# Kernel tuning notes

Measured on AMD Instinct MI355X. Metric: run time of the kernel, lower is better.

Reference implementation:

```python
import jax, jax.numpy as jnp
import numpy as np

D_MODEL = 512
N_HEADS = 8
D_HEAD = D_MODEL // N_HEADS  # 64


def setup_inputs() -> dict:
    key = jax.random.key(0)
    ks = jax.random.split(key, 9)
    S = 4096
    sc_qkv = 1.0 / np.sqrt(D_MODEL)
    x = jax.random.normal(ks[0], (S, D_MODEL), dtype=jnp.float32)
    # per-head projection weights, stacked over heads: [H, D_MODEL, D_HEAD]
    Wq = jax.random.normal(ks[1], (N_HEADS, D_MODEL, D_HEAD), dtype=jnp.float32) * sc_qkv
    Wk = jax.random.normal(ks[2], (N_HEADS, D_MODEL, D_HEAD), dtype=jnp.float32) * sc_qkv
    Wv = jax.random.normal(ks[3], (N_HEADS, D_MODEL, D_HEAD), dtype=jnp.float32) * sc_qkv
    bq = jax.random.normal(ks[4], (N_HEADS, D_HEAD), dtype=jnp.float32) * 0.01
    bk = jax.random.normal(ks[5], (N_HEADS, D_HEAD), dtype=jnp.float32) * 0.01
    bv = jax.random.normal(ks[6], (N_HEADS, D_HEAD), dtype=jnp.float32) * 0.01
    # output projection (nn.Linear(512,512)): weight [out,in], bias [out]
    Wo = jax.random.normal(ks[7], (D_MODEL, D_MODEL), dtype=jnp.float32) * sc_qkv
    bo = jax.random.normal(ks[8], (D_MODEL,), dtype=jnp.float32) * 0.01
    return {"x": x, "Wq": Wq, "Wk": Wk, "Wv": Wv, "bq": bq, "bk": bk, "bv": bv, "Wo": Wo, "bo": bo}


def reference(x, Wq, Wk, Wv, bq, bk, bv, Wo, bo):
    # x: [S, D_MODEL]; all heads batched in one einsum (replaces python loop)
    q = jnp.einsum('sd,hdk->hsk', x, Wq) + bq[:, None, :]  # [H,S,Dh]
    k = jnp.einsum('sd,hdk->hsk', x, Wk) + bk[:, None, :]
    v = jnp.einsum('sd,hdk->hsk', x, Wv) + bv[:, None, :]
    scale = 1.0 / jnp.sqrt(jnp.asarray(D_HEAD, dtype=q.dtype))
    scores = jnp.einsum('hsk,htk->hst', q, k) * scale  # [H,S,S]
    attn = jax.nn.softmax(scores, axis=-1)
    ctx = jnp.einsum('hst,htk->hsk', attn, v)  # [H,S,Dh]
    # concat heads along feature dim: [S, H*Dh] (head-major order matches torch.concat)
    S = x.shape[0]
    concat = jnp.transpose(ctx, (1, 0, 2)).reshape(S, N_HEADS * D_HEAD)
    # nn.Linear: y = x @ W^T + b
    return concat @ Wo.T + bo
```

## Files before the change

kernel.cpp:

```cpp
#include <hip/hip_runtime.h>

#define S 4096
#define DM 512
#define NH 8
#define DHD 64
#define KVSPLIT 2
#define KVLEN (S / KVSPLIT)
#define ALPHA 0.18033688011112042f

using short8 = __attribute__((ext_vector_type(8))) short;
using f32x4  = __attribute__((ext_vector_type(4))) float;

__device__ __forceinline__ unsigned short f2bf(float f) {
  union { float f; unsigned int u; } v; v.f = f;
  unsigned int r = v.u + 0x7FFF + ((v.u >> 16) & 1);
  return (unsigned short)(r >> 16);
}

__device__ __forceinline__ float bf2f(unsigned short u) {
  union { unsigned int u; float f; } v; v.u = (unsigned)u << 16;
  return v.f;
}

__device__ __forceinline__ unsigned int cvt_pk_bf16(float a, float b) {
  unsigned int r;
  asm("v_cvt_pk_bf16_f32 %0, %1, %2" : "=v"(r) : "v"(a), "v"(b));
  return r;
}

__device__ __forceinline__ void async16(void* lds, const void* g) {
  __builtin_amdgcn_global_load_lds((const __attribute__((address_space(1))) void*)g,
                                   (__attribute__((address_space(3))) void*)lds, 16, 0, 0);
}

__global__ void cvt2_f32_bf16(const float* __restrict__ a, unsigned short* __restrict__ da, int na,
                              const float* __restrict__ b, unsigned short* __restrict__ db, int nb) {
  int i = (blockIdx.x * 256 + threadIdx.x) * 4;
  const float* src; unsigned short* dst;
  if (i < na) { src = a + i; dst = da + i; }
  else { int j = i - na; if (j >= nb) return; src = b + j; dst = db + j; }
  float4 v = *(const float4*)src;
  uint2 o;
  o.x = (unsigned)f2bf(v.x) | ((unsigned)f2bf(v.y) << 16);
  o.y = (unsigned)f2bf(v.z) | ((unsigned)f2bf(v.w) << 16);
  *(uint2*)dst = o;
}

__global__ void pack_w(const float* __restrict__ Wq, const float* __restrict__ Wk,
                       const float* __restrict__ Wv, unsigned short* __restrict__ Wcat) {
  __shared__ float T[64][68];
  const int d0 = blockIdx.x * 64, h = blockIdx.y, t = blockIdx.z;
  const float* W = (t == 0 ? Wq : t == 1 ? Wk : Wv) + (size_t)h * DM * DHD;
  const int tid = threadIdx.x;
#pragma unroll
  for (int i = 0; i < 4; ++i) {
    int c = i * 256 + tid;
    int r = c >> 4, u = c & 15;
    *(float4*)&T[r][u * 4] = *(const float4*)&W[(size_t)(d0 + r) * DHD + u * 4];
  }
  __syncthreads();
#pragma unroll
  for (int i = 0; i < 2; ++i) {
    int c = i * 256 + tid;
    int dh = c >> 3, u = c & 7;
    unsigned short tmp[8];
#pragma unroll
    for (int j = 0; j < 8; ++j) tmp[j] = f2bf(T[u * 8 + j][dh]);
    *(uint4*)&Wcat[((size_t)(t * 512) + h * 64 + dh) * DM + d0 + u * 8] = *(uint4*)tmp;
  }
}

template <int EPI>
__global__ void __launch_bounds__(256, 2)
gemm_bt(const unsigned short* __restrict__ A,
        const unsigned short* __restrict__ B,
        int K,
        const float* __restrict__ b0, const float* __restrict__ b1, const float* __restrict__ b2,
        unsigned short* __restrict__ Qb, unsigned short* __restrict__ Kb, unsigned short* __restrict__ Vtb,
        float* __restrict__ outp) {
  __shared__ unsigned short As[128 * 32];
  __shared__ unsigned short Bs[128 * 32];
  const int tid = threadIdx.x;
  const int wid = tid >> 6, lane = tid & 63;
  const int lo = lane & 15, hi = lane >> 4;
  const int wr = wid >> 1, wc = wid & 1;
  const int m0 = blockIdx.x * 128, n0 = blockIdx.y * 128;
  f32x4 acc[4][4] = {};
  for (int k0 = 0; k0 < K; k0 += 32) {
    __syncthreads();
#pragma unroll
    for (int i = 0; i < 2; ++i) {
      const int cb = (wid * 2 + i) * 64;
      const int c = cb + lane;
      const int r = c >> 2, u = c & 3;
      async16(&As[cb * 8], A + (size_t)(m0 + r) * K + k0 + u * 8);
      async16(&Bs[cb * 8], B + (size_t)(n0 + r) * K + k0 + u * 8);
    }
    __syncthreads();
    short8 af[4], bfr[4];
#pragma unroll
    for (int m = 0; m < 4; ++m) af[m] = *(const short8*)&As[(wr * 64 + m * 16 + lo) * 32 + hi * 8];
#pragma unroll
    for (int n = 0; n < 4; ++n) bfr[n] = *(const short8*)&Bs[(wc * 64 + n * 16 + lo) * 32 + hi * 8];
#pragma unroll
    for (int m = 0; m < 4; ++m)
#pragma unroll
      for (int n = 0; n < 4; ++n)
        acc[m][n] = __builtin_amdgcn_mfma_f32_16x16x32_bf16(af[m], bfr[n], acc[m][n], 0, 0, 0);
  }
#pragma unroll
  for (int mi = 0; mi < 4; ++mi)
#pragma unroll
    for (int ni = 0; ni < 4; ++ni) {
      const int n = n0 + wc * 64 + ni * 16 + lo;
      const int mbase = m0 + wr * 64 + mi * 16 + hi * 4;
      if (EPI == 0) {
        const int t = n >> 9, h = (n >> 6) & 7, dh = n & 63;
        const float bias = (t == 0 ? b0 : t == 1 ? b1 : b2)[h * 64 + dh];
        if (t == 2) {
          unsigned short tmp[4];
#pragma unroll
          for (int r = 0; r < 4; ++r) tmp[r] = f2bf(acc[mi][ni][r] + bias);
          *(uint2*)&Vtb[((size_t)h * DHD + dh) * S + mbase] = *(uint2*)tmp;
        } else {
          unsigned short* dst = (t == 0 ? Qb : Kb);
#pragma unroll
          for (int r = 0; r < 4; ++r) {
            float v = acc[mi][ni][r] + bias;
            if (t == 0) v *= ALPHA;
            dst[((size_t)h * S + mbase + r) * DHD + dh] = f2bf(v);
          }
        }
      } else {
#pragma unroll
        for (int r = 0; r < 4; ++r)
          outp[(size_t)(mbase + r) * DM + n] = acc[mi][ni][r] + b0[n];
      }
    }
}

__global__ void __launch_bounds__(256, 4)
attn_kernel(const unsigned short* __restrict__ Qb, const unsigned short* __restrict__ Kb,
            const unsigned short* __restrict__ Vtb, unsigned short* __restrict__ accP,
            float2* __restrict__ lmP) {
  __shared__ unsigned short Ks[2][64 * 64];
  __shared__ unsigned short Vs[2][64 * 64];
  __shared__ unsigned short Ps[4][16 * 64];
  const int tid = threadIdx.x;
  const int wid = tid >> 6, lane = tid & 63;
  const int lo = lane & 15, hi = lane >> 4;
  const int h = blockIdx.y;
  const int q0 = blockIdx.x * 64;
  const int sp = blockIdx.z;
  const int kvbase = sp * KVLEN;
  const unsigned short* Qh  = Qb  + (size_t)h * S * DHD;
  const unsigned short* Kh  = Kb  + (size_t)h * S * DHD;
  const unsigned short* Vth = Vtb + (size_t)h * DHD * S;
  const int qrow = q0 + wid * 16 + lo;
  short8 qf[2];
#pragma unroll
  for (int kf = 0; kf < 2; ++kf)
    qf[kf] = *(const short8*)&Qh[(size_t)qrow * DHD + kf * 32 + hi * 8];

  float m_r = -__builtin_inff(), l_r = 0.f;
  f32x4 acc[4] = {};

  auto stage = [&](int b, int kv0) {
#pragma unroll
    for (int i = 0; i < 2; ++i) {
      const int cb = (wid * 2 + i) * 64;
      const int c = cb + lane;
      const int r = c >> 3, up = c & 7;
      const int u = up ^ (r & 7);
      async16(&Ks[b][cb * 8], Kh  + (size_t)(kv0 + r) * DHD + u * 8);
      async16(&Vs[b][cb * 8], Vth + (size_t)r * S + kv0 + u * 8);
    }
  };

  stage(0, kvbase);
  __syncthreads();
  int cur = 0;
  for (int kv0 = kvbase; kv0 < kvbase + KVLEN; kv0 += 64) {
    if (kv0 + 64 < kvbase + KVLEN) stage(cur ^ 1, kv0 + 64);
    f32x4 sc[4];
    __builtin_amdgcn_s_setprio(1);
#pragma unroll
    for (int ct = 0; ct < 4; ++ct) {
      sc[ct] = (f32x4){0.f, 0.f, 0.f, 0.f};
#pragma unroll
      for (int kf = 0; kf < 2; ++kf) {
        const int r = ct * 16 + lo;
        const int u = kf * 4 + hi;
        const short8 kfr = *(const short8*)&Ks[cur][r * 64 + (u ^ (r & 7)) * 8];
        sc[ct] = __builtin_amdgcn_mfma_f32_16x16x32_bf16(kfr, qf[kf], sc[ct], 0, 0, 0);
      }
    }
    __builtin_amdgcn_s_setprio(0);
    float pm = fmaxf(fmaxf(fmaxf(sc[0][0], sc[0][1]), fmaxf(sc[0][2], sc[0][3])),
                     fmaxf(fmaxf(sc[1][0], sc[1][1]), fmaxf(sc[1][2], sc[1][3])));
    pm = fmaxf(pm, fmaxf(fmaxf(fmaxf(sc[2][0], sc[2][1]), fmaxf(sc[2][2], sc[2][3])),
                         fmaxf(fmaxf(sc[3][0], sc[3][1]), fmaxf(sc[3][2], sc[3][3]))));
    pm = fmaxf(pm, __shfl_xor(pm, 16));
    pm = fmaxf(pm, __shfl_xor(pm, 32));
    if (__any(pm > m_r + 8.f)) {
      const float mn = fmaxf(m_r, pm);
      const float sca = exp2f(m_r - mn);
      m_r = mn;
      l_r *= sca;
#pragma unroll
      for (int dt = 0; dt < 4; ++dt)
#pragma unroll
        for (int r = 0; r < 4; ++r) acc[dt][r] *= sca;
    }
    float ps = 0.f;
#pragma unroll
    for (int ct = 0; ct < 4; ++ct)
#pragma unroll
      for (int r = 0; r < 4; ++r) {
        const float p = exp2f(sc[ct][r] - m_r);
        sc[ct][r] = p;
        ps += p;
      }
    ps += __shfl_xor(ps, 16);
    ps += __shfl_xor(ps, 32);
    l_r += ps;
    unsigned short* Pw = &Ps[wid][0];
    const int swz = (lo & 7) << 3;
#pragma unroll
    for (int ct = 0; ct < 4; ++ct) {
      uint2 w;
      w.x = cvt_pk_bf16(sc[ct][0], sc[ct][1]);
      w.y = cvt_pk_bf16(sc[ct][2], sc[ct][3]);
      *(uint2*)&Pw[lo * 64 + ((ct * 16 + hi * 4) ^ swz)] = w;
    }
    asm volatile("" ::: "memory");
    short8 pb[2];
#pragma unroll
    for (int kc = 0; kc < 2; ++kc)
      pb[kc] = *(const short8*)&Pw[lo * 64 + ((kc * 32 + hi * 8) ^ swz)];
    __builtin_amdgcn_s_setprio(1);
#pragma unroll
    for (int dt = 0; dt < 4; ++dt)
#pragma unroll
      for (int kc = 0; kc < 2; ++kc) {
        const int r2 = dt * 16 + lo;
        const int u = kc * 4 + hi;
        const short8 vf = *(const short8*)&Vs[cur][r2 * 64 + (u ^ (r2 & 7)) * 8];
        acc[dt] = __builtin_amdgcn_mfma_f32_16x16x32_bf16(vf, pb[kc], acc[dt], 0, 0, 0);
      }
    __builtin_amdgcn_s_setprio(0);
    __syncthreads();
    cur ^= 1;
  }
  const size_t prow = (size_t)(sp * NH + h) * S + qrow;
#pragma unroll
  for (int dt = 0; dt < 4; ++dt) {
    unsigned short tmp[4];
#pragma unroll
    for (int r = 0; r < 4; ++r) tmp[r] = f2bf(acc[dt][r]);
    *(uint2*)&accP[prow * 64 + dt * 16 + hi * 4] = *(uint2*)tmp;
  }
  if (hi == 0) lmP[prow] = make_float2(m_r, l_r);
}

__global__ void merge_kernel(const unsigned short* __restrict__ accP, const float2* __restrict__ lmP,
                             unsigned short* __restrict__ concat) {
  const int c = blockIdx.x * 256 + threadIdx.x;
  const int row = c >> 3;
  const int h = row >> 12, q = row & (S - 1);
  const int dh0 = (c & 7) * 8;
  const float2 lm0 = lmP[row];
  const float2 lm1 = lmP[NH * S + row];
  const float M = fmaxf(lm0.x, lm1.x);
  float w0 = exp2f(lm0.x - M), w1 = exp2f(lm1.x - M);
  const float inv = 1.f / (lm0.y * w0 + lm1.y * w1);
  w0 *= inv; w1 *= inv;
  const short8 v0 = *(const short8*)&accP[(size_t)row * 64 + dh0];
  const short8 v1 = *(const short8*)&accP[((size_t)NH * S + row) * 64 + dh0];
  unsigned short out[8];
#pragma unroll
  for (int j = 0; j < 8; ++j)
    out[j] = f2bf(bf2f((unsigned short)v0[j]) * w0 + bf2f((unsigned short)v1[j]) * w1);
  *(uint4*)&concat[(size_t)q * DM + h * DHD + dh0] = *(uint4*)out;
}

extern "C" void kernel_launch(void* const* d_in, const int* in_sizes, int n_in,
                              void* d_out, int out_size, void* d_ws, size_t ws_size,
                              hipStream_t stream) {
  const float* x  = (const float*)d_in[0];
  const float* Wq = (const float*)d_in[1];
  const float* Wk = (const float*)d_in[2];
  const float* Wv = (const float*)d_in[3];
  const float* bq = (const float*)d_in[4];
  const float* bk = (const float*)d_in[5];
  const float* bv = (const float*)d_in[6];
  const float* Wo = (const float*)d_in[7];
  const float* bo = (const float*)d_in[8];
  float* outp = (float*)d_out;
  char* ws = (char*)d_ws;
  unsigned short* Qbuf   = (unsigned short*)(ws + 0);
  unsigned short* Kbuf   = (unsigned short*)(ws + 4194304);
  unsigned short* Vtbuf  = (unsigned short*)(ws + 8388608);
  unsigned short* concat = (unsigned short*)(ws + 12582912);
  unsigned short* Wob    = (unsigned short*)(ws + 16777216);
  float2*         lmP    = (float2*)(ws + 17301504);
  unsigned short* xb     = (unsigned short*)(ws + 17825792);
  unsigned short* Wcat   = (unsigned short*)(ws + 22020096);
  unsigned short* accP   = (unsigned short*)(ws + 17825792);

  cvt2_f32_bf16<<<(S * DM + DM * DM) / 1024, 256, 0, stream>>>(x, xb, S * DM, Wo, Wob, DM * DM);
  pack_w<<<dim3(8, NH, 3), 256, 0, stream>>>(Wq, Wk, Wv, Wcat);
  gemm_bt<0><<<dim3(S / 128, 1536 / 128), 256, 0, stream>>>(xb, Wcat, DM, bq, bk, bv,
                                                            Qbuf, Kbuf, Vtbuf, nullptr);
  attn_kernel<<<dim3(S / 64, NH, KVSPLIT), 256, 0, stream>>>(Qbuf, Kbuf, Vtbuf, accP, lmP);
  merge_kernel<<<(NH * S * 8) / 256, 256, 0, stream>>>(accP, lmP, concat);
  gemm_bt<1><<<dim3(S / 128, DM / 128), 256, 0, stream>>>(concat, Wob, DM, bo, nullptr, nullptr,
                                                          nullptr, nullptr, nullptr, outp);
}
```

Measured before the change: 184.6 us.

## Switch attention to 32x32 MFMA with in-register P, fuse prep kernels, narrow GEMM tiles

The attention kernel moves from 16x16x32 to 32x32x16 bf16 MFMA tiles with 128 query rows per block. The P matrix is repacked in registers with v_permlane32_swap instead of going through LDS, which removes the per-wave LDS staging and its traffic. The two preprocessing kernels are merged into one launch, and the GEMM N-tile is halved to 64 with higher occupancy bounds to get more blocks in flight. The trade-offs are higher register pressure in attention (launch bounds lowered to 2) and less data reuse per GEMM tile.

```diff
diff --git a/kernel.cpp b/kernel.cpp
--- a/kernel.cpp
+++ b/kernel.cpp
@@ -10,6 +10,7 @@
 
 using short8 = __attribute__((ext_vector_type(8))) short;
 using f32x4  = __attribute__((ext_vector_type(4))) float;
+using f32x16 = __attribute__((ext_vector_type(16))) float;
 
 __device__ __forceinline__ unsigned short f2bf(float f) {
   union { float f; unsigned int u; } v; v.f = f;
@@ -28,30 +29,37 @@
   return r;
 }
 
+__device__ __forceinline__ void permswap(unsigned int& d, unsigned int& s) {
+  asm("v_permlane32_swap_b32 %0, %1" : "+v"(d), "+v"(s));
+}
+
 __device__ __forceinline__ void async16(void* lds, const void* g) {
   __builtin_amdgcn_global_load_lds((const __attribute__((address_space(1))) void*)g,
                                    (__attribute__((address_space(3))) void*)lds, 16, 0, 0);
 }
 
-__global__ void cvt2_f32_bf16(const float* __restrict__ a, unsigned short* __restrict__ da, int na,
-                              const float* __restrict__ b, unsigned short* __restrict__ db, int nb) {
-  int i = (blockIdx.x * 256 + threadIdx.x) * 4;
-  const float* src; unsigned short* dst;
-  if (i < na) { src = a + i; dst = da + i; }
-  else { int j = i - na; if (j >= nb) return; src = b + j; dst = db + j; }
-  float4 v = *(const float4*)src;
-  uint2 o;
-  o.x = (unsigned)f2bf(v.x) | ((unsigned)f2bf(v.y) << 16);
-  o.y = (unsigned)f2bf(v.z) | ((unsigned)f2bf(v.w) << 16);
-  *(uint2*)dst = o;
-}
-
-__global__ void pack_w(const float* __restrict__ Wq, const float* __restrict__ Wk,
-                       const float* __restrict__ Wv, unsigned short* __restrict__ Wcat) {
+#define NCVT ((S * DM + DM * DM) / 1024)
+__global__ void prep(const float* __restrict__ x, unsigned short* __restrict__ xb,
+                     const float* __restrict__ Wo, unsigned short* __restrict__ Wob,
+                     const float* __restrict__ Wq, const float* __restrict__ Wk,
+                     const float* __restrict__ Wv, unsigned short* __restrict__ Wcat) {
   __shared__ float T[64][68];
-  const int d0 = blockIdx.x * 64, h = blockIdx.y, t = blockIdx.z;
+  const int tid = threadIdx.x;
+  if (blockIdx.x < NCVT) {
+    int i = (blockIdx.x * 256 + tid) * 4;
+    const float* src; unsigned short* dst;
+    if (i < S * DM) { src = x + i; dst = xb + i; }
+    else { int j = i - S * DM; src = Wo + j; dst = Wob + j; }
+    float4 v = *(const float4*)src;
+    uint2 o;
+    o.x = (unsigned)f2bf(v.x) | ((unsigned)f2bf(v.y) << 16);
+    o.y = (unsigned)f2bf(v.z) | ((unsigned)f2bf(v.w) << 16);
+    *(uint2*)dst = o;
+    return;
+  }
+  const int bid = blockIdx.x - NCVT;
+  const int d0 = (bid & 7) * 64, h = (bid >> 3) & 7, t = bid >> 6;
   const float* W = (t == 0 ? Wq : t == 1 ? Wk : Wv) + (size_t)h * DM * DHD;
-  const int tid = threadIdx.x;
 #pragma unroll
   for (int i = 0; i < 4; ++i) {
     int c = i * 256 + tid;
@@ -71,7 +79,7 @@
 }
 
 template <int EPI>
-__global__ void __launch_bounds__(256, 2)
+__global__ void __launch_bounds__(256, 4)
 gemm_bt(const unsigned short* __restrict__ A,
         const unsigned short* __restrict__ B,
         int K,
@@ -79,40 +87,43 @@
         unsigned short* __restrict__ Qb, unsigned short* __restrict__ Kb, unsigned short* __restrict__ Vtb,
         float* __restrict__ outp) {
   __shared__ unsigned short As[128 * 32];
-  __shared__ unsigned short Bs[128 * 32];
+  __shared__ unsigned short Bs[64 * 32];
   const int tid = threadIdx.x;
   const int wid = tid >> 6, lane = tid & 63;
   const int lo = lane & 15, hi = lane >> 4;
   const int wr = wid >> 1, wc = wid & 1;
-  const int m0 = blockIdx.x * 128, n0 = blockIdx.y * 128;
-  f32x4 acc[4][4] = {};
+  const int m0 = blockIdx.x * 128, n0 = blockIdx.y * 64;
+  f32x4 acc[4][2] = {};
   for (int k0 = 0; k0 < K; k0 += 32) {
     __syncthreads();
 #pragma unroll
     for (int i = 0; i < 2; ++i) {
       const int cb = (wid * 2 + i) * 64;
-      const int c = cb + lane;
-      const int r = c >> 2, u = c & 3;
+      const int c = cb + lane, r = c >> 2, u = c & 3;
       async16(&As[cb * 8], A + (size_t)(m0 + r) * K + k0 + u * 8);
+    }
+    {
+      const int cb = wid * 64;
+      const int c = cb + lane, r = c >> 2, u = c & 3;
       async16(&Bs[cb * 8], B + (size_t)(n0 + r) * K + k0 + u * 8);
     }
     __syncthreads();
-    short8 af[4], bfr[4];
+    short8 af[4], bfr[2];
 #pragma unroll
     for (int m = 0; m < 4; ++m) af[m] = *(const short8*)&As[(wr * 64 + m * 16 + lo) * 32 + hi * 8];
 #pragma unroll
-    for (int n = 0; n < 4; ++n) bfr[n] = *(const short8*)&Bs[(wc * 64 + n * 16 + lo) * 32 + hi * 8];
+    for (int n = 0; n < 2; ++n) bfr[n] = *(const short8*)&Bs[(wc * 32 + n * 16 + lo) * 32 + hi * 8];
 #pragma unroll
     for (int m = 0; m < 4; ++m)
 #pragma unroll
-      for (int n = 0; n < 4; ++n)
+      for (int n = 0; n < 2; ++n)
         acc[m][n] = __builtin_amdgcn_mfma_f32_16x16x32_bf16(af[m], bfr[n], acc[m][n], 0, 0, 0);
   }
 #pragma unroll
   for (int mi = 0; mi < 4; ++mi)
 #pragma unroll
-    for (int ni = 0; ni < 4; ++ni) {
-      const int n = n0 + wc * 64 + ni * 16 + lo;
+    for (int ni = 0; ni < 2; ++ni) {
+      const int n = n0 + wc * 32 + ni * 16 + lo;
       const int mbase = m0 + wr * 64 + mi * 16 + hi * 4;
       if (EPI == 0) {
         const int t = n >> 9, h = (n >> 6) & 7, dh = n & 63;
@@ -139,41 +150,39 @@
     }
 }
 
-__global__ void __launch_bounds__(256, 4)
+__global__ void __launch_bounds__(256, 2)
 attn_kernel(const unsigned short* __restrict__ Qb, const unsigned short* __restrict__ Kb,
             const unsigned short* __restrict__ Vtb, unsigned short* __restrict__ accP,
             float2* __restrict__ lmP) {
   __shared__ unsigned short Ks[2][64 * 64];
   __shared__ unsigned short Vs[2][64 * 64];
-  __shared__ unsigned short Ps[4][16 * 64];
   const int tid = threadIdx.x;
   const int wid = tid >> 6, lane = tid & 63;
-  const int lo = lane & 15, hi = lane >> 4;
-  const int h = blockIdx.y;
-  const int q0 = blockIdx.x * 64;
-  const int sp = blockIdx.z;
+  const int l = lane & 31, b = lane >> 5;
+  const int h = blockIdx.y, sp = blockIdx.z;
+  const int q0 = blockIdx.x * 128;
   const int kvbase = sp * KVLEN;
   const unsigned short* Qh  = Qb  + (size_t)h * S * DHD;
   const unsigned short* Kh  = Kb  + (size_t)h * S * DHD;
   const unsigned short* Vth = Vtb + (size_t)h * DHD * S;
-  const int qrow = q0 + wid * 16 + lo;
-  short8 qf[2];
-#pragma unroll
-  for (int kf = 0; kf < 2; ++kf)
-    qf[kf] = *(const short8*)&Qh[(size_t)qrow * DHD + kf * 32 + hi * 8];
+  const int qrow = q0 + wid * 32 + l;
+  short8 qf[4];
+#pragma unroll
+  for (int ks = 0; ks < 4; ++ks)
+    qf[ks] = *(const short8*)&Qh[(size_t)qrow * DHD + ks * 16 + b * 8];
 
   float m_r = -__builtin_inff(), l_r = 0.f;
-  f32x4 acc[4] = {};
-
-  auto stage = [&](int b, int kv0) {
+  f32x16 acc[2] = {};
+
+  auto stage = [&](int bu, int kv0) {
 #pragma unroll
     for (int i = 0; i < 2; ++i) {
       const int cb = (wid * 2 + i) * 64;
       const int c = cb + lane;
       const int r = c >> 3, up = c & 7;
       const int u = up ^ (r & 7);
-      async16(&Ks[b][cb * 8], Kh  + (size_t)(kv0 + r) * DHD + u * 8);
-      async16(&Vs[b][cb * 8], Vth + (size_t)r * S + kv0 + u * 8);
+      async16(&Ks[bu][cb * 8], Kh  + (size_t)(kv0 + r) * DHD + u * 8);
+      async16(&Vs[bu][cb * 8], Vth + (size_t)r * S + kv0 + u * 8);
     }
   };
 
@@ -182,25 +191,28 @@
   int cur = 0;
   for (int kv0 = kvbase; kv0 < kvbase + KVLEN; kv0 += 64) {
     if (kv0 + 64 < kvbase + KVLEN) stage(cur ^ 1, kv0 + 64);
-    f32x4 sc[4];
+    f32x16 sc[2];
     __builtin_amdgcn_s_setprio(1);
 #pragma unroll
-    for (int ct = 0; ct < 4; ++ct) {
-      sc[ct] = (f32x4){0.f, 0.f, 0.f, 0.f};
-#pragma unroll
-      for (int kf = 0; kf < 2; ++kf) {
-        const int r = ct * 16 + lo;
-        const int u = kf * 4 + hi;
+    for (int t = 0; t < 2; ++t) {
+      sc[t] = (f32x16)0.0f;
+#pragma unroll
+      for (int ks = 0; ks < 4; ++ks) {
+        const int r = t * 32 + l;
+        const int u = ks * 2 + b;
         const short8 kfr = *(const short8*)&Ks[cur][r * 64 + (u ^ (r & 7)) * 8];
-        sc[ct] = __builtin_amdgcn_mfma_f32_16x16x32_bf16(kfr, qf[kf], sc[ct], 0, 0, 0);
+        sc[t] = __builtin_amdgcn_mfma_f32_32x32x16_bf16(kfr, qf[ks], sc[t], 0, 0, 0);
       }
     }
     __builtin_amdgcn_s_setprio(0);
-    float pm = fmaxf(fmaxf(fmaxf(sc[0][0], sc[0][1]), fmaxf(sc[0][2], sc[0][3])),
-                     fmaxf(fmaxf(sc[1][0], sc[1][1]), fmaxf(sc[1][2], sc[1][3])));
-    pm = fmaxf(pm, fmaxf(fmaxf(fmaxf(sc[2][0], sc[2][1]), fmaxf(sc[2][2], sc[2][3])),
-                         fmaxf(fmaxf(sc[3][0], sc[3][1]), fmaxf(sc[3][2], sc[3][3]))));
-    pm = fmaxf(pm, __shfl_xor(pm, 16));
+    float mx[16];
+#pragma unroll
+    for (int i = 0; i < 16; ++i) mx[i] = fmaxf(sc[0][i], sc[1][i]);
+#pragma unroll
+    for (int s2 = 8; s2 > 0; s2 >>= 1)
+#pragma unroll
+      for (int i = 0; i < 8; ++i) if (i < s2) mx[i] = fmaxf(mx[i], mx[i + s2]);
+    float pm = mx[0];
     pm = fmaxf(pm, __shfl_xor(pm, 32));
     if (__any(pm > m_r + 8.f)) {
       const float mn = fmaxf(m_r, pm);
@@ -208,59 +220,62 @@
       m_r = mn;
       l_r *= sca;
 #pragma unroll
-      for (int dt = 0; dt < 4; ++dt)
-#pragma unroll
-        for (int r = 0; r < 4; ++r) acc[dt][r] *= sca;
-    }
-    float ps = 0.f;
-#pragma unroll
-    for (int ct = 0; ct < 4; ++ct)
-#pragma unroll
-      for (int r = 0; r < 4; ++r) {
-        const float p = exp2f(sc[ct][r] - m_r);
-        sc[ct][r] = p;
-        ps += p;
-      }
-    ps += __shfl_xor(ps, 16);
+      for (int dt = 0; dt < 2; ++dt)
+#pragma unroll
+        for (int i = 0; i < 16; ++i) acc[dt][i] *= sca;
+    }
+#pragma unroll
+    for (int t = 0; t < 2; ++t)
+#pragma unroll
+      for (int i = 0; i < 16; ++i) sc[t][i] = exp2f(sc[t][i] - m_r);
+    float sm[16];
+#pragma unroll
+    for (int i = 0; i < 16; ++i) sm[i] = sc[0][i] + sc[1][i];
+#pragma unroll
+    for (int s2 = 8; s2 > 0; s2 >>= 1)
+#pragma unroll
+      for (int i = 0; i < 8; ++i) if (i < s2) sm[i] += sm[i + s2];
+    float ps = sm[0];
     ps += __shfl_xor(ps, 32);
     l_r += ps;
-    unsigned short* Pw = &Ps[wid][0];
-    const int swz = (lo & 7) << 3;
-#pragma unroll
-    for (int ct = 0; ct < 4; ++ct) {
-      uint2 w;
-      w.x = cvt_pk_bf16(sc[ct][0], sc[ct][1]);
-      w.y = cvt_pk_bf16(sc[ct][2], sc[ct][3]);
-      *(uint2*)&Pw[lo * 64 + ((ct * 16 + hi * 4) ^ swz)] = w;
-    }
-    asm volatile("" ::: "memory");
-    short8 pb[2];
-#pragma unroll
-    for (int kc = 0; kc < 2; ++kc)
-      pb[kc] = *(const short8*)&Pw[lo * 64 + ((kc * 32 + hi * 8) ^ swz)];
     __builtin_amdgcn_s_setprio(1);
 #pragma unroll
-    for (int dt = 0; dt < 4; ++dt)
-#pragma unroll
-      for (int kc = 0; kc < 2; ++kc) {
-        const int r2 = dt * 16 + lo;
-        const int u = kc * 4 + hi;
-        const short8 vf = *(const short8*)&Vs[cur][r2 * 64 + (u ^ (r2 & 7)) * 8];
-        acc[dt] = __builtin_amdgcn_mfma_f32_16x16x32_bf16(vf, pb[kc], acc[dt], 0, 0, 0);
+    for (int t = 0; t < 2; ++t) {
+      unsigned int pk[8];
+#pragma unroll
+      for (int i = 0; i < 8; ++i) pk[i] = cvt_pk_bf16(sc[t][2 * i], sc[t][2 * i + 1]);
+#pragma unroll
+      for (int kse = 0; kse < 2; ++kse) {
+        unsigned int a0 = pk[4 * kse + 0], a1 = pk[4 * kse + 1];
+        unsigned int c0 = pk[4 * kse + 2], c1 = pk[4 * kse + 3];
+        permswap(a0, c0);
+        permswap(a1, c1);
+        uint4 pw = make_uint4(a0, a1, c0, c1);
+        const short8 pb = *(const short8*)&pw;
+        const int ks = t * 2 + kse;
+#pragma unroll
+        for (int dt = 0; dt < 2; ++dt) {
+          const int r2 = dt * 32 + l;
+          const int u = ks * 2 + b;
+          const short8 vf = *(const short8*)&Vs[cur][r2 * 64 + (u ^ (r2 & 7)) * 8];
+          acc[dt] = __builtin_amdgcn_mfma_f32_32x32x16_bf16(vf, pb, acc[dt], 0, 0, 0);
+        }
       }
+    }
     __builtin_amdgcn_s_setprio(0);
     __syncthreads();
     cur ^= 1;
   }
   const size_t prow = (size_t)(sp * NH + h) * S + qrow;
 #pragma unroll
-  for (int dt = 0; dt < 4; ++dt) {
-    unsigned short tmp[4];
-#pragma unroll
-    for (int r = 0; r < 4; ++r) tmp[r] = f2bf(acc[dt][r]);
-    *(uint2*)&accP[prow * 64 + dt * 16 + hi * 4] = *(uint2*)tmp;
-  }
-  if (hi == 0) lmP[prow] = make_float2(m_r, l_r);
+  for (int dt = 0; dt < 2; ++dt)
+#pragma unroll
+    for (int qd = 0; qd < 4; ++qd) {
+      unsigned int w0 = cvt_pk_bf16(acc[dt][4 * qd + 0], acc[dt][4 * qd + 1]);
+      unsigned int w1 = cvt_pk_bf16(acc[dt][4 * qd + 2], acc[dt][4 * qd + 3]);
+      *(uint2*)&accP[prow * 64 + dt * 32 + qd * 8 + b * 4] = make_uint2(w0, w1);
+    }
+  if (b == 0) lmP[prow] = make_float2(m_r, l_r);
 }
 
 __global__ void merge_kernel(const unsigned short* __restrict__ accP, const float2* __restrict__ lmP,
@@ -308,12 +323,11 @@
   unsigned short* Wcat   = (unsigned short*)(ws + 22020096);
   unsigned short* accP   = (unsigned short*)(ws + 17825792);
 
-  cvt2_f32_bf16<<<(S * DM + DM * DM) / 1024, 256, 0, stream>>>(x, xb, S * DM, Wo, Wob, DM * DM);
-  pack_w<<<dim3(8, NH, 3), 256, 0, stream>>>(Wq, Wk, Wv, Wcat);
-  gemm_bt<0><<<dim3(S / 128, 1536 / 128), 256, 0, stream>>>(xb, Wcat, DM, bq, bk, bv,
-                                                            Qbuf, Kbuf, Vtbuf, nullptr);
-  attn_kernel<<<dim3(S / 64, NH, KVSPLIT), 256, 0, stream>>>(Qbuf, Kbuf, Vtbuf, accP, lmP);
+  prep<<<NCVT + 192, 256, 0, stream>>>(x, xb, Wo, Wob, Wq, Wk, Wv, Wcat);
+  gemm_bt<0><<<dim3(S / 128, 1536 / 64), 256, 0, stream>>>(xb, Wcat, DM, bq, bk, bv,
+                                                           Qbuf, Kbuf, Vtbuf, nullptr);
+  attn_kernel<<<dim3(S / 128, NH, KVSPLIT), 256, 0, stream>>>(Qbuf, Kbuf, Vtbuf, accP, lmP);
   merge_kernel<<<(NH * S * 8) / 256, 256, 0, stream>>>(accP, lmP, concat);
-  gemm_bt<1><<<dim3(S / 128, DM / 128), 256, 0, stream>>>(concat, Wob, DM, bo, nullptr, nullptr,
-                                                          nullptr, nullptr, nullptr, outp);
-}
+  gemm_bt<1><<<dim3(S / 128, DM / 64), 256, 0, stream>>>(concat, Wob, DM, bo, nullptr, nullptr,
+                                                         nullptr, nullptr, nullptr, outp);
+}
```

After: 174.1 us. 5.7% less time.
